# Performance work log

Measured on AMD Instinct MI355X. Metric: run time of the kernel, lower is better.

## Reference

```python
import jax, jax.numpy as jnp
import numpy as np

B, L, D, K, H = 2, 384, 1024, 128, 32
NUM_EDGES = 25600
NUM_T = 1000
SCALING = K ** -0.5
SQRT_2PI = float(np.sqrt(2.0 * np.pi))


def setup_inputs() -> dict:
    key = jax.random.key(0)
    ks = jax.random.split(key, 20)
    s = 0.02
    inp = {}
    inp["token_id"] = jax.random.randint(ks[0], (B, L), 0, 160)
    inp["is_periodic"] = jnp.zeros((B,), dtype=bool)
    inp["pos"] = 5.0 * jax.random.normal(ks[1], (B, L, 3), dtype=jnp.float32)
    inp["adj"] = jnp.ones((B, L, L), dtype=bool)
    inp["node_type_edge"] = jax.random.randint(ks[2], (B, L, L, 2), 0, NUM_EDGES)
    inp["time_step"] = jax.random.uniform(ks[3], (B, L), dtype=jnp.float32)
    inp["clean_mask"] = jnp.zeros((B, L), dtype=bool)
    # parameters
    inp["embed_w"] = s * jax.random.normal(ks[4], (160, D), dtype=jnp.float32)
    inp["Wpos"] = s * jax.random.normal(ks[5], (K, 3), dtype=jnp.float32)
    inp["Wpfe"] = s * jax.random.normal(ks[6], (D, K), dtype=jnp.float32)
    inp["gbf_means"] = jax.random.normal(ks[7], (K,), dtype=jnp.float32)
    inp["gbf_stds"] = 0.5 + jax.random.uniform(ks[8], (K,), dtype=jnp.float32)
    inp["gbf_mul"] = 1.0 + s * jax.random.normal(ks[9], (NUM_EDGES, 1), dtype=jnp.float32)
    inp["gbf_bias"] = s * jax.random.normal(ks[10], (NUM_EDGES, 1), dtype=jnp.float32)
    inp["W1"] = s * jax.random.normal(ks[11], (K, K), dtype=jnp.float32)
    inp["b1"] = jnp.zeros((K,), dtype=jnp.float32)
    inp["W2"] = s * jax.random.normal(ks[12], (H, K), dtype=jnp.float32)
    inp["b2"] = jnp.zeros((H,), dtype=jnp.float32)
    inp["Wproj"] = s * jax.random.normal(ks[13], (D, K), dtype=jnp.float32)
    inp["bproj"] = jnp.zeros((D,), dtype=jnp.float32)
    inp["Wt1"] = s * jax.random.normal(ks[14], (D, D), dtype=jnp.float32)
    inp["bt1"] = jnp.zeros((D,), dtype=jnp.float32)
    inp["Wt2"] = s * jax.random.normal(ks[15], (D, D), dtype=jnp.float32)
    inp["bt2"] = jnp.zeros((D,), dtype=jnp.float32)
    return inp


def _forward(token_id, is_periodic, pos, adj, node_type_edge, time_step, clean_mask,
             embed_w, Wpos, Wpfe, gbf_means, gbf_stds, gbf_mul, gbf_bias,
             W1, b1, W2, b2, Wproj, bproj, Wt1, bt1, Wt2, bt2):
    padding_mask = token_id == 0                                  # (B,L)
    molecule_mask = (token_id <= 129) & (~is_periodic[:, None])   # (B,L)
    x = embed_w[token_id]                                         # (B,L,D)

    # ---- _pos_emb (non-PBC branch: expand_pos = pos, expand_mask = padding_mask) ----
    delta = pos[:, :, None, :] - pos[:, None, :, :]               # (B,L,L,3)
    dist = jnp.sqrt(jnp.maximum(jnp.sum(delta * delta, -1), 1e-12))  # (B,L,L), safe norm

    # GaussianLayer
    mul = gbf_mul[node_type_edge].sum(-2)                         # (B,L,L,1)
    bias = gbf_bias[node_type_edge].sum(-2)                       # (B,L,L,1)
    y = mul * dist[..., None] + bias                              # (B,L,L,1) -> broadcast K
    std = jnp.abs(gbf_stds) + 1e-5
    a = (y - gbf_means) / std
    edge_feature = jnp.exp(-0.5 * a * a) / (SQRT_2PI * std)       # (B,L,L,K)

    # NonLinear projection to per-head bias
    gab = jax.nn.gelu(edge_feature @ W1.T + b1, approximate=False) @ W2.T + b2  # (B,L,L,H)
    gab = jnp.where(padding_mask[:, None, :, None], -jnp.inf, gab)  # expand-col mask
    gab = jnp.where(padding_mask[:, :, None, None], 0.0, gab)       # padding-row mask
    pos_attn_bias = jnp.transpose(gab, (0, 3, 1, 2))              # (B,H,L,L)

    d = gab.sum(-1)                                               # (B,L,L) sum over heads
    minv = jnp.finfo(jnp.float32).min
    d = jnp.where(padding_mask[:, None, :], minv, d)
    d = jnp.where(padding_mask[:, :, None], minv, d)
    adj_eff = adj | (~molecule_mask[:, :, None])
    d = jnp.where(~adj_eff, minv, d)
    attn = jax.nn.softmax(d * SCALING, axis=-1)                   # (B,L,L)

    pos_e = pos @ Wpos.T                                          # (B,L,K)
    pos_e = jnp.where(padding_mask[..., None], 0.0, pos_e)
    pfe = jnp.einsum('bij,bjk->bik', attn, pos_e)                 # (B,L,K)
    pfe = pfe @ Wpfe.T                                            # (B,L,D)

    ef = jnp.where(padding_mask[:, None, :, None], 0.0, edge_feature).sum(-2)  # (B,L,K)
    pfe = pfe + ef @ Wproj.T + bproj
    pos_embedding = jnp.where(padding_mask[..., None], 0.0, pfe)  # (B,L,D)

    # ---- time step encoder (sinusoidal + MLP) ----
    t = jnp.where(clean_mask, 0.0, time_step) * NUM_T             # (B,L)
    half = D // 2
    freqs = jnp.exp(-jnp.log(10000.0) * jnp.arange(half, dtype=jnp.float32) / half)
    ang = t[..., None] * freqs                                    # (B,L,half)
    sin_emb = jnp.concatenate([jnp.sin(ang), jnp.cos(ang)], -1)   # (B,L,D)
    time_embed = jax.nn.silu(sin_emb @ Wt1.T + bt1) @ Wt2.T + bt2

    x = x + time_embed + pos_embedding
    return x, padding_mask, time_embed, pos_attn_bias, pos_embedding


def reference(token_id, is_periodic, pos, adj, node_type_edge, time_step, clean_mask,
              embed_w, Wpos, Wpfe, gbf_means, gbf_stds, gbf_mul, gbf_bias,
              W1, b1, W2, b2, Wproj, bproj, Wt1, bt1, Wt2, bt2):
    return _forward(token_id, is_periodic, pos, adj, node_type_edge, time_step, clean_mask,
                    embed_w, Wpos, Wpfe, gbf_means, gbf_stds, gbf_mul, gbf_bias,
                    W1, b1, W2, b2, Wproj, bproj, Wt1, bt1, Wt2, bt2)
```

## Files before the change

kernel.cpp:

```cpp
#include <hip/hip_runtime.h>
#include <stddef.h>

#define B_ 2
#define L_ 384
#define D_ 1024
#define K_ 128
#define H_ 32

#define MINV (-3.402823466e38f)
#define NEG_BIG (-1.0e38f)
#define SCALING_ 0.08838834764831845f
#define INV_SQRT_2PI 0.3989422804014327f

typedef __attribute__((ext_vector_type(8))) short bf16x8;
typedef __attribute__((ext_vector_type(4))) float f32x4;

__device__ __forceinline__ float finitize(float x) {
    return fminf(fmaxf(x, -1.0e38f), 1.0e38f);
}
__device__ __forceinline__ unsigned short f2bf(float x) {
    unsigned int u = __float_as_uint(x);
    u += 0x7FFFu + ((u >> 16) & 1u);
    return (unsigned short)(u >> 16);
}
__device__ __forceinline__ unsigned short f2bf_rtz(float x) {
    return (unsigned short)(__float_as_uint(x) >> 16);
}
__device__ __forceinline__ float gelu_tanh(float x) {
    const float x2 = x * x;
    const float z = x * fmaf(0.0356774081f, x2, 0.7978845608f);
    const float e = __expf(2.0f * z);
    const float t = fmaf(-2.0f, __builtin_amdgcn_rcpf(e + 1.0f), 1.0f);
    const float hx = 0.5f * x;
    return fmaf(hx, t, hx);
}

__global__ __launch_bounds__(256) void prep_sin_kernel(
    const float* __restrict__ W1, const float* __restrict__ W2,
    const float* __restrict__ Wpfe, const float* __restrict__ Wproj,
    unsigned short* __restrict__ W1bf, unsigned short* __restrict__ W2bf,
    unsigned short* __restrict__ Wpfebf, unsigned short* __restrict__ Wprojbf,
    const float* __restrict__ time_step, const unsigned char* __restrict__ clean,
    const int* __restrict__ token, unsigned short* __restrict__ sin_bf,
    float* __restrict__ padout)
{
    const int blk = blockIdx.x;
    if (blk < 276) {
        const int i = blk * 256 + threadIdx.x;
        if (i >= 70656) return;
        const float* src; unsigned short* dst; int off;
        if (i < 4096)       { src = W1;    dst = W1bf;    off = i; }
        else if (i < 5120)  { src = W2;    dst = W2bf;    off = i - 4096; }
        else if (i < 37888) { src = Wpfe;  dst = Wpfebf;  off = i - 5120; }
        else                { src = Wproj; dst = Wprojbf; off = i - 37888; }
        const float4 v = ((const float4*)src)[off];
        ushort4 p; p.x = f2bf(v.x); p.y = f2bf(v.y); p.z = f2bf(v.z); p.w = f2bf(v.w);
        ((ushort4*)dst)[off] = p;
    } else {
        const int row = blk - 276;
        if (threadIdx.x == 0) padout[row] = (token[row] == 0) ? 1.0f : 0.0f;
        const float t = (clean[row] ? 0.0f : time_step[row]) * 1000.0f;
        for (int k = threadIdx.x; k < 512; k += 256) {
            const float f = __expf(-9.210340371976184f * (float)k * (1.0f / 512.0f));
            const float ang = t * f;
            sin_bf[(size_t)row * D_ + k]       = f2bf(__sinf(ang));
            sin_bf[(size_t)row * D_ + 512 + k] = f2bf(__cosf(ang));
        }
    }
}

__device__ __forceinline__ void gemm_ts_body(
    char* smem, int m0, int n0,
    const unsigned short* __restrict__ A, const float* __restrict__ Bw,
    const float* __restrict__ bias, void* __restrict__ Cv,
    int N, int Kd, int act, f32x4* accOut)
{
    unsigned short (*sA)[72] = (unsigned short(*)[72])smem;
    unsigned short (*sB)[72] = (unsigned short(*)[72])(smem + 4608);
    const int tid  = threadIdx.x;
    const int lane = tid & 63;
    const int wave = tid >> 6;
    const int l15  = lane & 15;
    const int quad = lane >> 4;
    const int mt   = wave & 1;
    const int np   = wave >> 1;

    const int ar = tid >> 3, ac = (tid & 7) * 8;
    const int bc4 = (tid & 15) * 4;

    f32x4 acc[2];
#pragma unroll
    for (int t = 0; t < 2; ++t) acc[t] = (f32x4){0.f, 0.f, 0.f, 0.f};

    uint4 ra = *(const uint4*)&A[(size_t)(m0 + ar) * Kd + ac];
    float4 rbv[4];
#pragma unroll
    for (int c = 0; c < 4; ++c)
        rbv[c] = *(const float4*)&Bw[(size_t)(n0 + ((tid + c * 256) >> 4)) * Kd + bc4];

    for (int k0 = 0; k0 < Kd; k0 += 64) {
        *(uint4*)&sA[ar][ac] = ra;
#pragma unroll
        for (int c = 0; c < 4; ++c) {
            ushort4 p;
            p.x = f2bf(rbv[c].x); p.y = f2bf(rbv[c].y);
            p.z = f2bf(rbv[c].z); p.w = f2bf(rbv[c].w);
            *(ushort4*)&sB[(tid + c * 256) >> 4][bc4] = p;
        }
        __syncthreads();
        if (k0 + 64 < Kd) {
            ra = *(const uint4*)&A[(size_t)(m0 + ar) * Kd + k0 + 64 + ac];
#pragma unroll
            for (int c = 0; c < 4; ++c)
                rbv[c] = *(const float4*)&Bw[(size_t)(n0 + ((tid + c * 256) >> 4)) * Kd + k0 + 64 + bc4];
        }
#pragma unroll
        for (int kk = 0; kk < 64; kk += 32) {
            const bf16x8 av = *(const bf16x8*)&sA[mt * 16 + l15][kk + quad * 8];
#pragma unroll
            for (int t = 0; t < 2; ++t) {
                const bf16x8 bv = *(const bf16x8*)&sB[(np * 2 + t) * 16 + l15][kk + quad * 8];
                acc[t] = __builtin_amdgcn_mfma_f32_16x16x32_bf16(av, bv, acc[t], 0, 0, 0);
            }
        }
        __syncthreads();
    }
    if (accOut) {
        accOut[0] = acc[0];
        accOut[1] = acc[1];
        return;
    }
#pragma unroll
    for (int t = 0; t < 2; ++t) {
        const int nc = n0 + (np * 2 + t) * 16 + l15;
        const float bv = bias[nc];
#pragma unroll
        for (int r = 0; r < 4; ++r) {
            const int mr = m0 + mt * 16 + quad * 4 + r;
            float v = acc[t][r] + bv;
            if (act) {
                v = v / (1.0f + __expf(-v));
                ((unsigned short*)Cv)[(size_t)mr * N + nc] = f2bf(v);
            } else {
                ((float*)Cv)[(size_t)mr * N + nc] = v;
            }
        }
    }
}

__device__ __forceinline__ void edge_body(
    char* smem, int row,
    const int* __restrict__ token_id,
    const unsigned char* __restrict__ is_periodic,
    const float* __restrict__ pos,
    const unsigned char* __restrict__ adj,
    const int* __restrict__ nte,
    const float* __restrict__ gbf_means,
    const float* __restrict__ gbf_stds,
    const float* __restrict__ gbf_mul,
    const float* __restrict__ gbf_bias,
    const float* __restrict__ b1,
    const float* __restrict__ b2,
    const float* __restrict__ Wpos,
    const unsigned short* __restrict__ W1bf,
    const unsigned short* __restrict__ W2bf,
    unsigned short* __restrict__ pfe_bf,
    unsigned short* __restrict__ ef_bf,
    float* __restrict__ out_pab)
{
    const int b = row / L_;
    const int i = row - b * L_;
    const int tid = threadIdx.x;

    const int tok_i = token_id[row];
    if (tok_i == 0) {
        for (int idx = tid; idx < H_ * L_; idx += 256) {
            const int h = idx / L_;
            const int j = idx - h * L_;
            out_pab[((size_t)(b * H_ + h) * L_ + i) * L_ + j] = 0.0f;
        }
        if (tid < K_) {
            pfe_bf[(size_t)row * K_ + tid] = 0;
            ef_bf[(size_t)row * K_ + tid]  = 0;
        }
        return;
    }

    typedef unsigned short efbuf_t[32][136];
    efbuf_t* sEF = (efbuf_t*)smem;
    unsigned short (*sACT)[136] = (unsigned short(*)[136])(smem + 17408);
    float (*sGab)[33] = (float(*)[33])(smem + 26112);
    float* sD      = (float*)(smem + 30336);
    float* sRed    = (float*)(smem + 31872);
    float* sYall   = (float*)(smem + 32896);
    unsigned char* sPadCol = (unsigned char*)(smem + 34432);

    for (int j = tid; j < L_; j += 256)
        sPadCol[j] = (token_id[b * L_ + j] == 0) ? 1 : 0;

    const float px = pos[(size_t)row * 3 + 0];
    const float py = pos[(size_t)row * 3 + 1];
    const float pz = pos[(size_t)row * 3 + 2];
    for (int jg2 = tid; jg2 < L_; jg2 += 256) {
        const float dx = px - pos[(size_t)(b * L_ + jg2) * 3 + 0];
        const float dy = py - pos[(size_t)(b * L_ + jg2) * 3 + 1];
        const float dz = pz - pos[(size_t)(b * L_ + jg2) * 3 + 2];
        const float dist = sqrtf(fmaxf(dx * dx + dy * dy + dz * dz, 1e-12f));
        const size_t eoff = ((size_t)(b * L_ + i) * L_ + jg2) * 2;
        const int e0 = nte[eoff], e1 = nte[eoff + 1];
        sYall[jg2] = (gbf_mul[e0] + gbf_mul[e1]) * dist + (gbf_bias[e0] + gbf_bias[e1]);
    }

    const int lane = tid & 63;
    const int wave = tid >> 6;
    const int l15  = lane & 15;
    const int quad = lane >> 4;
    const int mt   = wave & 1;
    const int ntb  = (wave >> 1) * 4;
    float rb1[4];
#pragma unroll
    for (int nt = 0; nt < 4; ++nt) rb1[nt] = b1[(ntb + nt) * 16 + l15];
    const int hc = (wave >> 1) * 16 + l15;
    const float rb2 = b2[hc];
    bf16x8 w1f[4][4];
#pragma unroll
    for (int ks = 0; ks < 4; ++ks)
#pragma unroll
        for (int nt = 0; nt < 4; ++nt)
            w1f[ks][nt] = *(const bf16x8*)&W1bf[((ntb + nt) * 16 + l15) * K_ + ks * 32 + quad * 8];
    bf16x8 bv2[4];
#pragma unroll
    for (int ks = 0; ks < 4; ++ks)
        bv2[ks] = *(const bf16x8*)&W2bf[hc * K_ + ks * 32 + quad * 8];

    const int kg4 = (tid & 31) * 4;
    const int jg  = tid >> 5;
    const int jb  = jg * 4;
    float meanv[4], istdv[4], cKv[4];
#pragma unroll
    for (int c = 0; c < 4; ++c) {
        meanv[c] = gbf_means[kg4 + c];
        const float s = fabsf(gbf_stds[kg4 + c]) + 1e-5f;
        istdv[c] = 1.0f / s;
        cKv[c]   = INV_SQRT_2PI * istdv[c];
    }
    float efs[4] = {0.f, 0.f, 0.f, 0.f};

    __syncthreads();

#pragma unroll
    for (int jj = 0; jj < 4; ++jj) {
        const int j = jb + jj;
        const float y = sYall[j];
        const bool ok = !sPadCol[j];
        ushort4 p;
#pragma unroll
        for (int c = 0; c < 4; ++c) {
            const float a = (y - meanv[c]) * istdv[c];
            const float ef = __expf(-0.5f * a * a) * cKv[c];
            ((unsigned short*)&p)[c] = f2bf_rtz(ef);
            if (ok) efs[c] += ef;
        }
        *(ushort4*)&sEF[0][j][kg4] = p;
    }
    __syncthreads();

    for (int tile = 0; tile < L_ / 32; ++tile) {
        const int jt0 = tile * 32;
        const int cur = tile & 1, nxt = cur ^ 1;

        f32x4 acc1[4];
#pragma unroll
        for (int nt = 0; nt < 4; ++nt) acc1[nt] = (f32x4){0.f, 0.f, 0.f, 0.f};
#pragma unroll
        for (int ks = 0; ks < 4; ++ks) {
            const bf16x8 av = *(const bf16x8*)&sEF[cur][mt * 16 + l15][ks * 32 + quad * 8];
#pragma unroll
            for (int nt = 0; nt < 4; ++nt)
                acc1[nt] = __builtin_amdgcn_mfma_f32_16x16x32_bf16(av, w1f[ks][nt], acc1[nt], 0, 0, 0);
        }

        if (tile + 1 < L_ / 32) {
            const int jn0 = jt0 + 32;
#pragma unroll
            for (int jj = 0; jj < 4; ++jj) {
                const int j = jb + jj;
                const float y = sYall[jn0 + j];
                const bool ok = !sPadCol[jn0 + j];
                ushort4 p;
#pragma unroll
                for (int c = 0; c < 4; ++c) {
                    const float a = (y - meanv[c]) * istdv[c];
                    const float ef = __expf(-0.5f * a * a) * cKv[c];
                    ((unsigned short*)&p)[c] = f2bf_rtz(ef);
                    if (ok) efs[c] += ef;
                }
                *(ushort4*)&sEF[nxt][j][kg4] = p;
            }
        }

#pragma unroll
        for (int nt = 0; nt < 4; ++nt) {
            const int kkc = (ntb + nt) * 16 + l15;
#pragma unroll
            for (int r = 0; r < 4; ++r) {
                const float v = gelu_tanh(acc1[nt][r] + rb1[nt]);
                sACT[mt * 16 + quad * 4 + r][kkc] = f2bf_rtz(v);
            }
        }
        __syncthreads();

        f32x4 acc2 = (f32x4){0.f, 0.f, 0.f, 0.f};
#pragma unroll
        for (int ks = 0; ks < 4; ++ks) {
            const bf16x8 av = *(const bf16x8*)&sACT[mt * 16 + l15][ks * 32 + quad * 8];
            acc2 = __builtin_amdgcn_mfma_f32_16x16x32_bf16(av, bv2[ks], acc2, 0, 0, 0);
        }
        const int jl0 = mt * 16 + quad * 4;
#pragma unroll
        for (int r = 0; r < 4; ++r) sGab[jl0 + r][hc] = acc2[r] + rb2;
        __syncthreads();

        {
            const int h = tid >> 3, f = tid & 7;
            const int jb2 = f * 4;
            float4 st;
#pragma unroll
            for (int r = 0; r < 4; ++r) {
                float v = finitize(sGab[jb2 + r][h]);
                if (sPadCol[jt0 + jb2 + r]) v = NEG_BIG;
                ((float*)&st)[r] = v;
            }
            *(float4*)&out_pab[((size_t)(b * H_ + h) * L_ + i) * L_ + jt0 + jb2] = st;
        }
        if (tid < 32) {
            float s = 0.0f;
#pragma unroll
            for (int h = 0; h < 32; ++h) s += sGab[tid][h];
            sD[jt0 + tid] = s;
        }
    }

    {
        float* efScr = (float*)sACT;
#pragma unroll
        for (int c = 0; c < 4; ++c) efScr[jg * 128 + kg4 + c] = efs[c];
    }
    __syncthreads();
    if (tid < 128) {
        const float* efScr = (const float*)sACT;
        float s = 0.0f;
#pragma unroll
        for (int g = 0; g < 8; ++g) s += efScr[g * 128 + tid];
        ef_bf[(size_t)row * K_ + tid] = f2bf(s);
    }
    __syncthreads();

    const bool molecule = (tok_i <= 129) && (is_periodic[b] == 0);
    float lmax = -INFINITY;
    for (int j = tid; j < L_; j += 256) {
        const bool colpad = sPadCol[j] != 0;
        const bool adj_eff = (adj[((size_t)(b * L_ + i)) * L_ + j] != 0) || (!molecule);
        const float dv = (colpad || !adj_eff) ? MINV : sD[j];
        const float s = dv * SCALING_;
        sD[j] = s;
        lmax = fmaxf(lmax, s);
    }
#pragma unroll
    for (int off = 32; off > 0; off >>= 1) lmax = fmaxf(lmax, __shfl_xor(lmax, off));
    if (lane == 0) sRed[wave] = lmax;
    __syncthreads();
    const float smax = fmaxf(fmaxf(sRed[0], sRed[1]), fmaxf(sRed[2], sRed[3]));
    float lsum = 0.0f;
    for (int j = tid; j < L_; j += 256) {
        const float e = __expf(sD[j] - smax);
        sD[j] = e;
        lsum += e;
    }
#pragma unroll
    for (int off = 32; off > 0; off >>= 1) lsum += __shfl_xor(lsum, off);
    if (lane == 0) sRed[4 + wave] = lsum;
    __syncthreads();
    const float inv = 1.0f / (sRed[4] + sRed[5] + sRed[6] + sRed[7]);

    float a0 = 0.f, a1 = 0.f, a2 = 0.f;
    for (int j = tid; j < L_; j += 256) {
        if (!sPadCol[j]) {
            const float e = sD[j];
            a0 += e * pos[(size_t)(b * L_ + j) * 3 + 0];
            a1 += e * pos[(size_t)(b * L_ + j) * 3 + 1];
            a2 += e * pos[(size_t)(b * L_ + j) * 3 + 2];
        }
    }
#pragma unroll
    for (int off = 32; off > 0; off >>= 1) {
        a0 += __shfl_xor(a0, off);
        a1 += __shfl_xor(a1, off);
        a2 += __shfl_xor(a2, off);
    }
    if (lane == 0) { sRed[8 + wave] = a0; sRed[12 + wave] = a1; sRed[16 + wave] = a2; }
    __syncthreads();
    if (tid < 128) {
        const float m0 = sRed[8] + sRed[9] + sRed[10] + sRed[11];
        const float m1 = sRed[12] + sRed[13] + sRed[14] + sRed[15];
        const float m2 = sRed[16] + sRed[17] + sRed[18] + sRed[19];
        const float w0 = Wpos[tid * 3 + 0], w1 = Wpos[tid * 3 + 1], w2 = Wpos[tid * 3 + 2];
        pfe_bf[(size_t)row * K_ + tid] = f2bf((m0 * w0 + m1 * w1 + m2 * w2) * inv);
    }
}

__global__ __launch_bounds__(256, 3) void edge_ts1(
    const int* __restrict__ token_id,
    const unsigned char* __restrict__ is_periodic,
    const float* __restrict__ pos,
    const unsigned char* __restrict__ adj,
    const int* __restrict__ nte,
    const float* __restrict__ gbf_means,
    const float* __restrict__ gbf_stds,
    const float* __restrict__ gbf_mul,
    const float* __restrict__ gbf_bias,
    const float* __restrict__ b1,
    const float* __restrict__ b2,
    const float* __restrict__ Wpos,
    const unsigned short* __restrict__ W1bf,
    const unsigned short* __restrict__ W2bf,
    unsigned short* __restrict__ pfe_bf,
    unsigned short* __restrict__ ef_bf,
    float* __restrict__ out_pab,
    const unsigned short* __restrict__ sin_bf,
    const float* __restrict__ Wt1,
    const float* __restrict__ bt1,
    unsigned short* __restrict__ h1_bf)
{
    __shared__ __align__(16) char smem[34816];
    const int bx = blockIdx.x;
    if (bx < B_ * L_) {
        edge_body(smem, bx, token_id, is_periodic, pos, adj, nte,
                  gbf_means, gbf_stds, gbf_mul, gbf_bias, b1, b2, Wpos,
                  W1bf, W2bf, pfe_bf, ef_bf, out_pab);
    } else {
        const int tsb = bx - B_ * L_;
        const int m0 = (tsb >> 4) * 32;
        const int n0 = (tsb & 15) * 64;
        gemm_ts_body(smem, m0, n0, sin_bf, Wt1, bt1, (void*)h1_bf, D_, D_, 1, nullptr);
    }
}

__global__ __launch_bounds__(256) void ts2_pe_kernel(
    const unsigned short* __restrict__ h1_bf,
    const float* __restrict__ Wt2,
    const float* __restrict__ bt2,
    const unsigned short* __restrict__ pfe_bf,
    const unsigned short* __restrict__ ef_bf,
    const unsigned short* __restrict__ Wpfebf,
    const unsigned short* __restrict__ Wprojbf,
    const float* __restrict__ bproj,
    const int* __restrict__ token,
    const float* __restrict__ embed_w,
    float* __restrict__ outTE,
    float* __restrict__ outPE,
    float* __restrict__ outX)
{
    __shared__ __align__(16) char smem[26112];
    const int tid  = threadIdx.x;
    const int lane = tid & 63;
    const int wave = tid >> 6;
    const int l15  = lane & 15;
    const int quad = lane >> 4;
    const int mt   = wave & 1;
    const int np   = wave >> 1;
    const int m0 = blockIdx.y * 32, n0 = blockIdx.x * 64;

    f32x4 accTE[2];
    gemm_ts_body(smem, m0, n0, h1_bf, Wt2, bt2, nullptr, D_, D_, 0, accTE);

    unsigned short (*sA2)[136] = (unsigned short(*)[136])smem;
    unsigned short (*sB2)[136] = (unsigned short(*)[136])(smem + 8704);
    f32x4 accPE[2];
#pragma unroll
    for (int t = 0; t < 2; ++t) accPE[t] = (f32x4){0.f, 0.f, 0.f, 0.f};

    for (int phase = 0; phase < 2; ++phase) {
        const unsigned short* Ap = phase ? ef_bf : pfe_bf;
        const unsigned short* Bp = phase ? Wprojbf : Wpfebf;
#pragma unroll
        for (int e = tid; e < 512; e += 256) {
            const int r = e >> 4, c8 = (e & 15) * 8;
            *(uint4*)&sA2[r][c8] = *(const uint4*)&Ap[(size_t)(m0 + r) * K_ + c8];
        }
#pragma unroll
        for (int e = tid; e < 1024; e += 256) {
            const int r = e >> 4, c8 = (e & 15) * 8;
            *(uint4*)&sB2[r][c8] = *(const uint4*)&Bp[(size_t)(n0 + r) * K_ + c8];
        }
        __syncthreads();
#pragma unroll
        for (int ks = 0; ks < 4; ++ks) {
            const bf16x8 av = *(const bf16x8*)&sA2[mt * 16 + l15][ks * 32 + quad * 8];
#pragma unroll
            for (int t = 0; t < 2; ++t) {
                const bf16x8 bv = *(const bf16x8*)&sB2[(np * 2 + t) * 16 + l15][ks * 32 + quad * 8];
                accPE[t] = __builtin_amdgcn_mfma_f32_16x16x32_bf16(av, bv, accPE[t], 0, 0, 0);
            }
        }
        __syncthreads();
    }

#pragma unroll
    for (int t = 0; t < 2; ++t) {
        const int nc = n0 + (np * 2 + t) * 16 + l15;
        const float bte = bt2[nc];
        const float bpe = bproj[nc];
#pragma unroll
        for (int r = 0; r < 4; ++r) {
            const int mr = m0 + mt * 16 + quad * 4 + r;
            const int tok = token[mr];
            const float te = accTE[t][r] + bte;
            const float pe = (tok == 0) ? 0.0f : (accPE[t][r] + bpe);
            outTE[(size_t)mr * D_ + nc] = te;
            outPE[(size_t)mr * D_ + nc] = pe;
            outX[(size_t)mr * D_ + nc] = embed_w[(size_t)tok * D_ + nc] + te + pe;
        }
    }
}

extern "C" void kernel_launch(void* const* d_in, const int* in_sizes, int n_in,
                              void* d_out, int out_size, void* d_ws, size_t ws_size,
                              hipStream_t stream) {
    const int*           token_id    = (const int*)d_in[0];
    const unsigned char* is_periodic = (const unsigned char*)d_in[1];
    const float*         pos         = (const float*)d_in[2];
    const unsigned char* adj         = (const unsigned char*)d_in[3];
    const int*           nte         = (const int*)d_in[4];
    const float*         time_step   = (const float*)d_in[5];
    const unsigned char* clean_mask  = (const unsigned char*)d_in[6];
    const float*         embed_w     = (const float*)d_in[7];
    const float*         Wpos        = (const float*)d_in[8];
    const float*         Wpfe        = (const float*)d_in[9];
    const float*         gbf_means   = (const float*)d_in[10];
    const float*         gbf_stds    = (const float*)d_in[11];
    const float*         gbf_mul     = (const float*)d_in[12];
    const float*         gbf_bias    = (const float*)d_in[13];
    const float*         W1          = (const float*)d_in[14];
    const float*         b1          = (const float*)d_in[15];
    const float*         W2          = (const float*)d_in[16];
    const float*         b2          = (const float*)d_in[17];
    const float*         Wproj       = (const float*)d_in[18];
    const float*         bproj       = (const float*)d_in[19];
    const float*         Wt1         = (const float*)d_in[20];
    const float*         bt1         = (const float*)d_in[21];
    const float*         Wt2         = (const float*)d_in[22];
    const float*         bt2         = (const float*)d_in[23];

    float* out = (float*)d_out;
    float* out_x   = out;
    float* out_pad = out + 786432;
    float* out_te  = out + 787200;
    float* out_pab = out + 1573632;
    float* out_pe  = out + 11010816;

    unsigned short* wsu = (unsigned short*)d_ws;
    unsigned short* W1bf    = wsu;
    unsigned short* W2bf    = wsu + 16384;
    unsigned short* Wpfebf  = wsu + 20480;
    unsigned short* Wprojbf = wsu + 151552;
    unsigned short* sin_bf  = wsu + 282624;
    unsigned short* h1_bf   = wsu + 1069056;
    unsigned short* pfe_bf  = wsu + 1855488;
    unsigned short* ef_bf   = wsu + 1953792;

    prep_sin_kernel<<<dim3(1044), dim3(256), 0, stream>>>(
        W1, W2, Wpfe, Wproj, W1bf, W2bf, Wpfebf, Wprojbf,
        time_step, clean_mask, token_id, sin_bf, out_pad);
    edge_ts1<<<dim3(B_ * L_ + 384), dim3(256), 0, stream>>>(
        token_id, is_periodic, pos, adj, nte, gbf_means, gbf_stds, gbf_mul, gbf_bias,
        b1, b2, Wpos, W1bf, W2bf, pfe_bf, ef_bf, out_pab,
        sin_bf, Wt1, bt1, h1_bf);
    ts2_pe_kernel<<<dim3(16, 24), dim3(256), 0, stream>>>(
        h1_bf, Wt2, bt2, pfe_bf, ef_bf, Wpfebf, Wprojbf, bproj, token_id, embed_w,
        out_te, out_pe, out_x);
}
```

Measured before the change: 188.1 us.

## Remove prep kernel by fusing weight casts and sinusoid generation into consumers

Drops the separate prep kernel that converted weights to bf16 and wrote the sinusoidal time embedding to workspace. Edge blocks now convert W1/W2 to bf16 on load and write the padding mask, the time GEMM computes sin/cos directly into its A tile, and the final kernel converts Wpfe/Wproj fp32 tiles on the fly. This removes one launch and the workspace round trip for the sinusoid. In exchange, transcendentals are recomputed per column tile and the fp32 weights are loaded at twice the bytes.

```diff
diff --git a/kernel.cpp b/kernel.cpp
--- a/kernel.cpp
+++ b/kernel.cpp
@@ -25,6 +25,14 @@
 }
 __device__ __forceinline__ unsigned short f2bf_rtz(float x) {
     return (unsigned short)(__float_as_uint(x) >> 16);
+}
+__device__ __forceinline__ bf16x8 cvt8(const float* __restrict__ p) {
+    const float4 a = *(const float4*)p;
+    const float4 b = *(const float4*)(p + 4);
+    union { unsigned short u[8]; bf16x8 v; } r;
+    r.u[0] = f2bf(a.x); r.u[1] = f2bf(a.y); r.u[2] = f2bf(a.z); r.u[3] = f2bf(a.w);
+    r.u[4] = f2bf(b.x); r.u[5] = f2bf(b.y); r.u[6] = f2bf(b.z); r.u[7] = f2bf(b.w);
+    return r.v;
 }
 __device__ __forceinline__ float gelu_tanh(float x) {
     const float x2 = x * x;
@@ -33,40 +41,6 @@
     const float t = fmaf(-2.0f, __builtin_amdgcn_rcpf(e + 1.0f), 1.0f);
     const float hx = 0.5f * x;
     return fmaf(hx, t, hx);
-}
-
-__global__ __launch_bounds__(256) void prep_sin_kernel(
-    const float* __restrict__ W1, const float* __restrict__ W2,
-    const float* __restrict__ Wpfe, const float* __restrict__ Wproj,
-    unsigned short* __restrict__ W1bf, unsigned short* __restrict__ W2bf,
-    unsigned short* __restrict__ Wpfebf, unsigned short* __restrict__ Wprojbf,
-    const float* __restrict__ time_step, const unsigned char* __restrict__ clean,
-    const int* __restrict__ token, unsigned short* __restrict__ sin_bf,
-    float* __restrict__ padout)
-{
-    const int blk = blockIdx.x;
-    if (blk < 276) {
-        const int i = blk * 256 + threadIdx.x;
-        if (i >= 70656) return;
-        const float* src; unsigned short* dst; int off;
-        if (i < 4096)       { src = W1;    dst = W1bf;    off = i; }
-        else if (i < 5120)  { src = W2;    dst = W2bf;    off = i - 4096; }
-        else if (i < 37888) { src = Wpfe;  dst = Wpfebf;  off = i - 5120; }
-        else                { src = Wproj; dst = Wprojbf; off = i - 37888; }
-        const float4 v = ((const float4*)src)[off];
-        ushort4 p; p.x = f2bf(v.x); p.y = f2bf(v.y); p.z = f2bf(v.z); p.w = f2bf(v.w);
-        ((ushort4*)dst)[off] = p;
-    } else {
-        const int row = blk - 276;
-        if (threadIdx.x == 0) padout[row] = (token[row] == 0) ? 1.0f : 0.0f;
-        const float t = (clean[row] ? 0.0f : time_step[row]) * 1000.0f;
-        for (int k = threadIdx.x; k < 512; k += 256) {
-            const float f = __expf(-9.210340371976184f * (float)k * (1.0f / 512.0f));
-            const float ang = t * f;
-            sin_bf[(size_t)row * D_ + k]       = f2bf(__sinf(ang));
-            sin_bf[(size_t)row * D_ + 512 + k] = f2bf(__cosf(ang));
-        }
-    }
 }
 
 __device__ __forceinline__ void gemm_ts_body(
@@ -148,6 +122,91 @@
     }
 }
 
+__device__ __forceinline__ void ts1_body(
+    char* smem, int m0, int n0,
+    const float* __restrict__ time_step,
+    const unsigned char* __restrict__ clean,
+    const float* __restrict__ Wt1,
+    const float* __restrict__ bt1,
+    unsigned short* __restrict__ h1_bf)
+{
+    unsigned short (*sA)[72] = (unsigned short(*)[72])smem;
+    unsigned short (*sB)[72] = (unsigned short(*)[72])(smem + 4608);
+    const int tid  = threadIdx.x;
+    const int lane = tid & 63;
+    const int wave = tid >> 6;
+    const int l15  = lane & 15;
+    const int quad = lane >> 4;
+    const int mt   = wave & 1;
+    const int np   = wave >> 1;
+
+    const int ar = tid >> 3, ac = (tid & 7) * 8;
+    const int bc4 = (tid & 15) * 4;
+    const int mra = m0 + ar;
+    const float tval = (clean[mra] ? 0.0f : time_step[mra]) * 1000.0f;
+    const float Lc = -9.210340371976184f * (1.0f / 512.0f);
+
+    f32x4 acc[2];
+#pragma unroll
+    for (int t = 0; t < 2; ++t) acc[t] = (f32x4){0.f, 0.f, 0.f, 0.f};
+
+    float4 rbv[4];
+#pragma unroll
+    for (int c = 0; c < 4; ++c)
+        rbv[c] = *(const float4*)&Wt1[(size_t)(n0 + ((tid + c * 256) >> 4)) * D_ + bc4];
+
+    for (int k0 = 0; k0 < D_; k0 += 64) {
+        {
+            union { unsigned short u[8]; uint4 q; } pk;
+            const int cbase = k0 + ac;
+            const bool issin = (cbase < 512);
+            const int cb0 = issin ? cbase : (cbase - 512);
+#pragma unroll
+            for (int cc = 0; cc < 8; ++cc) {
+                const float f = __expf(Lc * (float)(cb0 + cc));
+                const float ang = tval * f;
+                pk.u[cc] = f2bf(issin ? __sinf(ang) : __cosf(ang));
+            }
+            *(uint4*)&sA[ar][ac] = pk.q;
+        }
+#pragma unroll
+        for (int c = 0; c < 4; ++c) {
+            ushort4 p;
+            p.x = f2bf(rbv[c].x); p.y = f2bf(rbv[c].y);
+            p.z = f2bf(rbv[c].z); p.w = f2bf(rbv[c].w);
+            *(ushort4*)&sB[(tid + c * 256) >> 4][bc4] = p;
+        }
+        __syncthreads();
+        if (k0 + 64 < D_) {
+#pragma unroll
+            for (int c = 0; c < 4; ++c)
+                rbv[c] = *(const float4*)&Wt1[(size_t)(n0 + ((tid + c * 256) >> 4)) * D_ + k0 + 64 + bc4];
+        }
+#pragma unroll
+        for (int kk = 0; kk < 64; kk += 32) {
+            const bf16x8 av = *(const bf16x8*)&sA[mt * 16 + l15][kk + quad * 8];
+#pragma unroll
+            for (int t = 0; t < 2; ++t) {
+                const bf16x8 bv = *(const bf16x8*)&sB[(np * 2 + t) * 16 + l15][kk + quad * 8];
+                acc[t] = __builtin_amdgcn_mfma_f32_16x16x32_bf16(av, bv, acc[t], 0, 0, 0);
+            }
+        }
+        __syncthreads();
+    }
+#pragma unroll
+    for (int t = 0; t < 2; ++t) {
+        const int nc = n0 + (np * 2 + t) * 16 + l15;
+        const float bv = bt1[nc];
+#pragma unroll
+        for (int r = 0; r < 4; ++r) {
+            const int mr = m0 + mt * 16 + quad * 4 + r;
+            float v = acc[t][r] + bv;
+            v = v / (1.0f + __expf(-v));
+            h1_bf[(size_t)mr * D_ + nc] = f2bf(v);
+        }
+    }
+}
+
 __device__ __forceinline__ void edge_body(
     char* smem, int row,
     const int* __restrict__ token_id,
@@ -162,17 +221,19 @@
     const float* __restrict__ b1,
     const float* __restrict__ b2,
     const float* __restrict__ Wpos,
-    const unsigned short* __restrict__ W1bf,
-    const unsigned short* __restrict__ W2bf,
+    const float* __restrict__ W1,
+    const float* __restrict__ W2,
     unsigned short* __restrict__ pfe_bf,
     unsigned short* __restrict__ ef_bf,
-    float* __restrict__ out_pab)
+    float* __restrict__ out_pab,
+    float* __restrict__ padout)
 {
     const int b = row / L_;
     const int i = row - b * L_;
     const int tid = threadIdx.x;
 
     const int tok_i = token_id[row];
+    if (tid == 0) padout[row] = (tok_i == 0) ? 1.0f : 0.0f;
     if (tok_i == 0) {
         for (int idx = tid; idx < H_ * L_; idx += 256) {
             const int h = idx / L_;
@@ -227,11 +288,11 @@
     for (int ks = 0; ks < 4; ++ks)
 #pragma unroll
         for (int nt = 0; nt < 4; ++nt)
-            w1f[ks][nt] = *(const bf16x8*)&W1bf[((ntb + nt) * 16 + l15) * K_ + ks * 32 + quad * 8];
+            w1f[ks][nt] = cvt8(&W1[(size_t)((ntb + nt) * 16 + l15) * K_ + ks * 32 + quad * 8]);
     bf16x8 bv2[4];
 #pragma unroll
     for (int ks = 0; ks < 4; ++ks)
-        bv2[ks] = *(const bf16x8*)&W2bf[hc * K_ + ks * 32 + quad * 8];
+        bv2[ks] = cvt8(&W2[(size_t)hc * K_ + ks * 32 + quad * 8]);
 
     const int kg4 = (tid & 31) * 4;
     const int jg  = tid >> 5;
@@ -422,12 +483,14 @@
     const float* __restrict__ b1,
     const float* __restrict__ b2,
     const float* __restrict__ Wpos,
-    const unsigned short* __restrict__ W1bf,
-    const unsigned short* __restrict__ W2bf,
+    const float* __restrict__ W1,
+    const float* __restrict__ W2,
     unsigned short* __restrict__ pfe_bf,
     unsigned short* __restrict__ ef_bf,
     float* __restrict__ out_pab,
-    const unsigned short* __restrict__ sin_bf,
+    float* __restrict__ padout,
+    const float* __restrict__ time_step,
+    const unsigned char* __restrict__ clean,
     const float* __restrict__ Wt1,
     const float* __restrict__ bt1,
     unsigned short* __restrict__ h1_bf)
@@ -437,12 +500,12 @@
     if (bx < B_ * L_) {
         edge_body(smem, bx, token_id, is_periodic, pos, adj, nte,
                   gbf_means, gbf_stds, gbf_mul, gbf_bias, b1, b2, Wpos,
-                  W1bf, W2bf, pfe_bf, ef_bf, out_pab);
+                  W1, W2, pfe_bf, ef_bf, out_pab, padout);
     } else {
         const int tsb = bx - B_ * L_;
         const int m0 = (tsb >> 4) * 32;
         const int n0 = (tsb & 15) * 64;
-        gemm_ts_body(smem, m0, n0, sin_bf, Wt1, bt1, (void*)h1_bf, D_, D_, 1, nullptr);
+        ts1_body(smem, m0, n0, time_step, clean, Wt1, bt1, h1_bf);
     }
 }
 
@@ -452,8 +515,8 @@
     const float* __restrict__ bt2,
     const unsigned short* __restrict__ pfe_bf,
     const unsigned short* __restrict__ ef_bf,
-    const unsigned short* __restrict__ Wpfebf,
-    const unsigned short* __restrict__ Wprojbf,
+    const float* __restrict__ Wpfe,
+    const float* __restrict__ Wproj,
     const float* __restrict__ bproj,
     const int* __restrict__ token,
     const float* __restrict__ embed_w,
@@ -482,16 +545,18 @@
 
     for (int phase = 0; phase < 2; ++phase) {
         const unsigned short* Ap = phase ? ef_bf : pfe_bf;
-        const unsigned short* Bp = phase ? Wprojbf : Wpfebf;
+        const float* Bpf = phase ? Wproj : Wpfe;
 #pragma unroll
         for (int e = tid; e < 512; e += 256) {
             const int r = e >> 4, c8 = (e & 15) * 8;
             *(uint4*)&sA2[r][c8] = *(const uint4*)&Ap[(size_t)(m0 + r) * K_ + c8];
         }
 #pragma unroll
-        for (int e = tid; e < 1024; e += 256) {
-            const int r = e >> 4, c8 = (e & 15) * 8;
-            *(uint4*)&sB2[r][c8] = *(const uint4*)&Bp[(size_t)(n0 + r) * K_ + c8];
+        for (int e = tid; e < 2048; e += 256) {
+            const int r = e >> 5, c4 = (e & 31) * 4;
+            const float4 v = *(const float4*)&Bpf[(size_t)(n0 + r) * K_ + c4];
+            ushort4 p; p.x = f2bf(v.x); p.y = f2bf(v.y); p.z = f2bf(v.z); p.w = f2bf(v.w);
+            *(ushort4*)&sB2[r][c4] = p;
         }
         __syncthreads();
 #pragma unroll
@@ -560,23 +625,15 @@
     float* out_pe  = out + 11010816;
 
     unsigned short* wsu = (unsigned short*)d_ws;
-    unsigned short* W1bf    = wsu;
-    unsigned short* W2bf    = wsu + 16384;
-    unsigned short* Wpfebf  = wsu + 20480;
-    unsigned short* Wprojbf = wsu + 151552;
-    unsigned short* sin_bf  = wsu + 282624;
-    unsigned short* h1_bf   = wsu + 1069056;
-    unsigned short* pfe_bf  = wsu + 1855488;
-    unsigned short* ef_bf   = wsu + 1953792;
-
-    prep_sin_kernel<<<dim3(1044), dim3(256), 0, stream>>>(
-        W1, W2, Wpfe, Wproj, W1bf, W2bf, Wpfebf, Wprojbf,
-        time_step, clean_mask, token_id, sin_bf, out_pad);
+    unsigned short* h1_bf  = wsu;
+    unsigned short* pfe_bf = wsu + 786432;
+    unsigned short* ef_bf  = wsu + 884736;
+
     edge_ts1<<<dim3(B_ * L_ + 384), dim3(256), 0, stream>>>(
         token_id, is_periodic, pos, adj, nte, gbf_means, gbf_stds, gbf_mul, gbf_bias,
-        b1, b2, Wpos, W1bf, W2bf, pfe_bf, ef_bf, out_pab,
-        sin_bf, Wt1, bt1, h1_bf);
+        b1, b2, Wpos, W1, W2, pfe_bf, ef_bf, out_pab, out_pad,
+        time_step, clean_mask, Wt1, bt1, h1_bf);
     ts2_pe_kernel<<<dim3(16, 24), dim3(256), 0, stream>>>(
-        h1_bf, Wt2, bt2, pfe_bf, ef_bf, Wpfebf, Wprojbf, bproj, token_id, embed_w,
+        h1_bf, Wt2, bt2, pfe_bf, ef_bf, Wpfe, Wproj, bproj, token_id, embed_w,
         out_te, out_pe, out_x);
 }
```

Result: slower. 210.6 us (+12.0%).
